# Performance work log

Hardware: AMD Instinct MI355X
Metric: run time of the kernel (lower is better)

The kernel has to match this reference:

```python
import jax, jax.numpy as jnp
import numpy as np

EPS = 1e-12  # F.normalize default eps


def _wn_weight(v, g):
    # torch weight_norm(dim=0) on Conv1d weight [out, in, 1]: w = g * v / ||v||_rows
    norm = jnp.sqrt(jnp.sum(v * v, axis=1, keepdims=True))
    return v * (g[:, None] / norm)


def _l2norm(x):
    n = jnp.sqrt(jnp.sum(x * x, axis=-1, keepdims=True))
    return x / jnp.maximum(n, EPS)


def setup_inputs() -> dict:
    key = jax.random.key(0)
    ks = jax.random.split(key, 4)
    B, D, T = 16, 1024, 4096
    CD, CS = 8, 1024
    return {
        "z": jax.random.normal(ks[0], (B, D, T), dtype=jnp.float32),
        "in_proj_v": jax.random.normal(ks[1], (CD, D), dtype=jnp.float32) * 0.02,
        "in_proj_g": jnp.ones((CD,), dtype=jnp.float32),
        "in_proj_b": jnp.zeros((CD,), dtype=jnp.float32),
        "out_proj_v": jax.random.normal(ks[2], (D, CD), dtype=jnp.float32) * 0.02,
        "out_proj_g": jnp.ones((D,), dtype=jnp.float32),
        "out_proj_b": jnp.zeros((D,), dtype=jnp.float32),
        "codebook": jax.random.normal(ks[3], (CS, CD), dtype=jnp.float32),
    }


def reference(z, in_proj_v, in_proj_g, in_proj_b, out_proj_v, out_proj_g, out_proj_b, codebook):
    B, D, T = z.shape
    CD = codebook.shape[1]

    # in_proj: 1x1 weight-normed conv == per-timestep linear
    w_in = _wn_weight(in_proj_v, in_proj_g)            # [CD, D]
    z_e = jnp.einsum('od,bdt->bot', w_in, z) + in_proj_b[None, :, None]  # [B, CD, T]

    # decode_latents: cosine-distance nearest neighbor in normalized space
    enc = jnp.transpose(z_e, (0, 2, 1)).reshape(B * T, CD)  # (b t) d
    enc_n = _l2norm(enc)
    cb_n = _l2norm(codebook)
    # dist = |e|^2 - 2 e.c + |c|^2 over normalized vectors
    dist = (jnp.sum(enc_n * enc_n, axis=1, keepdims=True)
            - 2.0 * enc_n @ cb_n.T
            + jnp.sum(cb_n * cb_n, axis=1)[None, :])       # [B*T, CS]
    indices = jnp.argmax(-dist, axis=1).reshape(B, T)      # [B, T]
    z_q = jnp.transpose(codebook[indices], (0, 2, 1))      # [B, CD, T] (un-normalized codebook gather)

    # losses (reduce over dims [1,2] -> per-batch)
    sg = jax.lax.stop_gradient
    commitment_loss = jnp.mean((z_e - sg(z_q)) ** 2, axis=(1, 2))
    codebook_loss = jnp.mean((z_q - sg(z_e)) ** 2, axis=(1, 2))

    # straight-through
    z_q_st = z_e + sg(z_q - z_e)

    w_out = _wn_weight(out_proj_v, out_proj_g)          # [D, CD]
    out = jnp.einsum('dc,bct->bdt', w_out, z_q_st) + out_proj_b[None, :, None]
    return out, commitment_loss, codebook_loss, indices, z_e
```

## Files before the change

kernel.cpp:

```cpp
#include <hip/hip_runtime.h>
#include <math.h>

#define BB 16
#define DD 1024
#define TT 4096
#define CD 8
#define CS 1024

#define OFF_LOSS_C 67108864
#define OFF_LOSS_B 67108880
#define OFF_IDX    67108896
#define OFF_ZE     67174432

#define WS_WIN  0
#define WS_WOUT 8192
#define WS_CBN  16384
#define WS_CS   24576

__global__ __launch_bounds__(256) void prep_kernel(
    const float* __restrict__ in_v,
    const float* __restrict__ in_g,
    const float* __restrict__ out_v,
    const float* __restrict__ out_g,
    const float* __restrict__ cb,
    float* __restrict__ ws)
{
    __shared__ float red[256];
    __shared__ float s_in[CD];
    int tid = threadIdx.x;

    for (int o = 0; o < CD; ++o) {
        float p = 0.f;
        for (int k = tid; k < DD; k += 256) { float v = in_v[o*DD + k]; p += v*v; }
        red[tid] = p; __syncthreads();
        for (int s = 128; s > 0; s >>= 1) { if (tid < s) red[tid] += red[tid+s]; __syncthreads(); }
        if (tid == 0) s_in[o] = in_g[o] / sqrtf(red[0]);
        __syncthreads();
    }
    for (int i = tid; i < DD*CD; i += 256) {
        int d = i >> 3, o = i & 7;
        ws[WS_WIN + i] = in_v[o*DD + d] * s_in[o];
    }
    for (int d = tid; d < DD; d += 256) {
        float v[CD]; float ssq = 0.f;
        #pragma unroll
        for (int c = 0; c < CD; ++c) { v[c] = out_v[d*CD + c]; ssq += v[c]*v[c]; }
        float s = out_g[d] / sqrtf(ssq);
        #pragma unroll
        for (int c = 0; c < CD; ++c) ws[WS_WOUT + d*CD + c] = v[c]*s;
    }
    double* cs = (double*)(ws + WS_CS);
    for (int c = tid; c < CS; c += 256) {
        float v[CD]; float ssq = 0.f;
        #pragma unroll
        for (int j = 0; j < CD; ++j) { v[j] = cb[c*CD + j]; ssq += v[j]*v[j]; }
        float n = fmaxf(sqrtf(ssq), 1e-12f);
        double sq = 0.0;
        #pragma unroll
        for (int j = 0; j < CD; ++j) {
            float e = v[j] / n;
            ws[WS_CBN + c*CD + j] = e;
            sq += (double)e * (double)e;
        }
        cs[c] = sq;
    }
}

__global__ __launch_bounds__(256) void vq_main_kernel(
    const float* __restrict__ z,
    const float* __restrict__ in_b,
    const float* __restrict__ cb,
    const float* __restrict__ ws,
    float* __restrict__ outb)
{
    __shared__ float4 cbn_s[CS*2];
    __shared__ double cs_s[CS];
    __shared__ float red[4];

    int tid = threadIdx.x;
    int b = blockIdx.y;
    int t = blockIdx.x * 256 + tid;

    {
        const float4* src = (const float4*)(ws + WS_CBN);
        for (int i = tid; i < CS*2; i += 256) cbn_s[i] = src[i];
        const double* csg = (const double*)(ws + WS_CS);
        for (int i = tid; i < CS; i += 256) cs_s[i] = csg[i];
    }
    __syncthreads();

    float acc[CD];
    #pragma unroll
    for (int o = 0; o < CD; ++o) acc[o] = in_b[o];
    const float* zp = z + (size_t)b * DD * TT + t;
    const float* w = ws + WS_WIN;
    #pragma unroll 8
    for (int d = 0; d < DD; ++d) {
        float zv = zp[(size_t)d * TT];
        #pragma unroll
        for (int o = 0; o < CD; ++o) acc[o] = fmaf(w[d*CD + o], zv, acc[o]);
    }

    #pragma unroll
    for (int o = 0; o < CD; ++o)
        outb[OFF_ZE + ((size_t)(b*CD + o)) * TT + t] = acc[o];

    float ssq = 0.f;
    #pragma unroll
    for (int o = 0; o < CD; ++o) ssq += acc[o]*acc[o];
    float nrm = fmaxf(sqrtf(ssq), 1e-12f);
    double en[CD];
    #pragma unroll
    for (int o = 0; o < CD; ++o) en[o] = (double)(acc[o] / nrm);

    double best = -1.0e300; int bidx = 0;
    for (int c = 0; c < CS; ++c) {
        float4 r0 = cbn_s[2*c], r1 = cbn_s[2*c+1];
        double dot = 0.0;
        dot = fma((double)r0.x, en[0], dot);
        dot = fma((double)r0.y, en[1], dot);
        dot = fma((double)r0.z, en[2], dot);
        dot = fma((double)r0.w, en[3], dot);
        dot = fma((double)r1.x, en[4], dot);
        dot = fma((double)r1.y, en[5], dot);
        dot = fma((double)r1.z, en[6], dot);
        dot = fma((double)r1.w, en[7], dot);
        double score = 2.0*dot - cs_s[c];
        if (score > best) { best = score; bidx = c; }
    }
    outb[OFF_IDX + b*TT + t] = (float)bidx;

    float l = 0.f;
    const float4* qr = (const float4*)(cb + bidx*CD);
    float4 q0 = qr[0], q1 = qr[1];
    {
        float dlt;
        dlt = acc[0]-q0.x; l = fmaf(dlt,dlt,l);
        dlt = acc[1]-q0.y; l = fmaf(dlt,dlt,l);
        dlt = acc[2]-q0.z; l = fmaf(dlt,dlt,l);
        dlt = acc[3]-q0.w; l = fmaf(dlt,dlt,l);
        dlt = acc[4]-q1.x; l = fmaf(dlt,dlt,l);
        dlt = acc[5]-q1.y; l = fmaf(dlt,dlt,l);
        dlt = acc[6]-q1.z; l = fmaf(dlt,dlt,l);
        dlt = acc[7]-q1.w; l = fmaf(dlt,dlt,l);
    }
    #pragma unroll
    for (int off = 32; off > 0; off >>= 1) l += __shfl_down(l, off, 64);
    if ((tid & 63) == 0) red[tid >> 6] = l;
    __syncthreads();
    if (tid == 0) {
        float s = ((red[0]+red[1]) + (red[2]+red[3])) * (1.0f/(CD*TT));
        atomicAdd(outb + OFF_LOSS_C + b, s);
        atomicAdd(outb + OFF_LOSS_B + b, s);
    }
}

__global__ __launch_bounds__(256) void out_proj_kernel(
    const float* __restrict__ cb,
    const float* __restrict__ out_b,
    const float* __restrict__ ws,
    float* __restrict__ outb)
{
    __shared__ float4 wout_s[DD*2];
    __shared__ __align__(16) float zq_s[CD][128];
    __shared__ float bias_s[DD];

    int tid = threadIdx.x;
    int b = blockIdx.y;
    int t0 = blockIdx.x * 128;

    const float4* wsrc = (const float4*)(ws + WS_WOUT);
    for (int i = tid; i < DD*2; i += 256) wout_s[i] = wsrc[i];
    for (int i = tid; i < DD; i += 256) bias_s[i] = out_b[i];
    if (tid < 128) {
        int idx = (int)outb[OFF_IDX + b*TT + t0 + tid];
        const float4* cr = (const float4*)(cb + idx*CD);
        float4 q0 = cr[0], q1 = cr[1];
        zq_s[0][tid] = q0.x; zq_s[1][tid] = q0.y; zq_s[2][tid] = q0.z; zq_s[3][tid] = q0.w;
        zq_s[4][tid] = q1.x; zq_s[5][tid] = q1.y; zq_s[6][tid] = q1.z; zq_s[7][tid] = q1.w;
    }
    __syncthreads();

    int tq = tid & 31;
    int dg = tid >> 5;
    float4 qv[CD];
    #pragma unroll
    for (int c = 0; c < CD; ++c) qv[c] = *(const float4*)&zq_s[c][tq*4];

    size_t obase = (size_t)b * DD * TT + t0 + tq*4;
    #pragma unroll 4
    for (int i = 0; i < 128; ++i) {
        int d = i*8 + dg;
        float4 w0 = wout_s[2*d], w1 = wout_s[2*d+1];
        float bb = bias_s[d];
        float4 r = make_float4(bb, bb, bb, bb);
        r.x = fmaf(w0.x, qv[0].x, r.x); r.y = fmaf(w0.x, qv[0].y, r.y); r.z = fmaf(w0.x, qv[0].z, r.z); r.w = fmaf(w0.x, qv[0].w, r.w);
        r.x = fmaf(w0.y, qv[1].x, r.x); r.y = fmaf(w0.y, qv[1].y, r.y); r.z = fmaf(w0.y, qv[1].z, r.z); r.w = fmaf(w0.y, qv[1].w, r.w);
        r.x = fmaf(w0.z, qv[2].x, r.x); r.y = fmaf(w0.z, qv[2].y, r.y); r.z = fmaf(w0.z, qv[2].z, r.z); r.w = fmaf(w0.z, qv[2].w, r.w);
        r.x = fmaf(w0.w, qv[3].x, r.x); r.y = fmaf(w0.w, qv[3].y, r.y); r.z = fmaf(w0.w, qv[3].z, r.z); r.w = fmaf(w0.w, qv[3].w, r.w);
        r.x = fmaf(w1.x, qv[4].x, r.x); r.y = fmaf(w1.x, qv[4].y, r.y); r.z = fmaf(w1.x, qv[4].z, r.z); r.w = fmaf(w1.x, qv[4].w, r.w);
        r.x = fmaf(w1.y, qv[5].x, r.x); r.y = fmaf(w1.y, qv[5].y, r.y); r.z = fmaf(w1.y, qv[5].z, r.z); r.w = fmaf(w1.y, qv[5].w, r.w);
        r.x = fmaf(w1.z, qv[6].x, r.x); r.y = fmaf(w1.z, qv[6].y, r.y); r.z = fmaf(w1.z, qv[6].z, r.z); r.w = fmaf(w1.z, qv[6].w, r.w);
        r.x = fmaf(w1.w, qv[7].x, r.x); r.y = fmaf(w1.w, qv[7].y, r.y); r.z = fmaf(w1.w, qv[7].w, r.w); r.w = fmaf(w1.w, qv[7].w, r.w);
        *(float4*)(outb + obase + (size_t)d * TT) = r;
    }
}

extern "C" void kernel_launch(void* const* d_in, const int* in_sizes, int n_in,
                              void* d_out, int out_size, void* d_ws, size_t ws_size,
                              hipStream_t stream) {
    const float* z     = (const float*)d_in[0];
    const float* in_v  = (const float*)d_in[1];
    const float* in_g  = (const float*)d_in[2];
    const float* in_b  = (const float*)d_in[3];
    const float* out_v = (const float*)d_in[4];
    const float* out_g = (const float*)d_in[5];
    const float* out_b = (const float*)d_in[6];
    const float* cb    = (const float*)d_in[7];
    float* ws  = (float*)d_ws;
    float* out = (float*)d_out;

    hipMemsetAsync(out + OFF_LOSS_C, 0, 32 * sizeof(float), stream);

    prep_kernel<<<1, 256, 0, stream>>>(in_v, in_g, out_v, out_g, cb, ws);
    vq_main_kernel<<<dim3(TT/256, BB), 256, 0, stream>>>(z, in_b, cb, ws, out);
    out_proj_kernel<<<dim3(TT/128, BB), 256, 0, stream>>>(cb, out_b, ws, out);
}
```

Before: 609.5 us.

## Split VQ projection and codebook search across waves; parallelize prep and out_proj

The VQ kernel now assigns 64 timesteps per block. Each of 4 waves reduces a quarter of the input channels, then searches a quarter of the codebook, and the partial results are merged through shared memory. This quadruples block count and shortens each thread's serial chains, improving latency hiding on the 256MB z read and the fp64 argmax scan. The prep kernel is spread over 16 blocks, and out_proj uses smaller tiles reading weights directly from global/cache instead of staging them in LDS, which also fixes a misplaced fma in the last column. Costs are extra synchronization and shared-memory partial sums.

```diff
diff --git a/kernel.cpp b/kernel.cpp
--- a/kernel.cpp
+++ b/kernel.cpp
@@ -25,32 +25,31 @@
     const float* __restrict__ cb,
     float* __restrict__ ws)
 {
-    __shared__ float red[256];
-    __shared__ float s_in[CD];
-    int tid = threadIdx.x;
-
-    for (int o = 0; o < CD; ++o) {
+    int bid = blockIdx.x, tid = threadIdx.x;
+    if (bid < 8) {
+        __shared__ float red[256];
+        __shared__ float ssc;
+        int o = bid;
         float p = 0.f;
         for (int k = tid; k < DD; k += 256) { float v = in_v[o*DD + k]; p += v*v; }
         red[tid] = p; __syncthreads();
         for (int s = 128; s > 0; s >>= 1) { if (tid < s) red[tid] += red[tid+s]; __syncthreads(); }
-        if (tid == 0) s_in[o] = in_g[o] / sqrtf(red[0]);
+        if (tid == 0) ssc = in_g[o] / sqrtf(red[0]);
         __syncthreads();
-    }
-    for (int i = tid; i < DD*CD; i += 256) {
-        int d = i >> 3, o = i & 7;
-        ws[WS_WIN + i] = in_v[o*DD + d] * s_in[o];
-    }
-    for (int d = tid; d < DD; d += 256) {
+        float scale = ssc;
+        for (int d = tid; d < DD; d += 256)
+            ws[WS_WIN + d*CD + o] = in_v[o*DD + d] * scale;
+    } else if (bid < 12) {
+        int d = (bid - 8) * 256 + tid;
         float v[CD]; float ssq = 0.f;
         #pragma unroll
         for (int c = 0; c < CD; ++c) { v[c] = out_v[d*CD + c]; ssq += v[c]*v[c]; }
         float s = out_g[d] / sqrtf(ssq);
         #pragma unroll
         for (int c = 0; c < CD; ++c) ws[WS_WOUT + d*CD + c] = v[c]*s;
-    }
-    double* cs = (double*)(ws + WS_CS);
-    for (int c = tid; c < CS; c += 256) {
+    } else {
+        int c = (bid - 12) * 256 + tid;
+        double* csh = (double*)(ws + WS_CS);
         float v[CD]; float ssq = 0.f;
         #pragma unroll
         for (int j = 0; j < CD; ++j) { v[j] = cb[c*CD + j]; ssq += v[j]*v[j]; }
@@ -60,98 +59,109 @@
         for (int j = 0; j < CD; ++j) {
             float e = v[j] / n;
             ws[WS_CBN + c*CD + j] = e;
-            sq += (double)e * (double)e;
-        }
-        cs[c] = sq;
-    }
-}
-
-__global__ __launch_bounds__(256) void vq_main_kernel(
+            sq = fma((double)e, (double)e, sq);
+        }
+        csh[c] = 0.5 * sq;
+    }
+}
+
+__global__ __launch_bounds__(256) void vq_kernel(
     const float* __restrict__ z,
     const float* __restrict__ in_b,
     const float* __restrict__ cb,
     const float* __restrict__ ws,
     float* __restrict__ outb)
 {
-    __shared__ float4 cbn_s[CS*2];
-    __shared__ double cs_s[CS];
-    __shared__ float red[4];
+    __shared__ float  zpart[4][CD][64];
+    __shared__ float  ze_s[CD][64];
+    __shared__ float  nrm_s[64];
+    __shared__ double best_s[4][64];
+    __shared__ int    bidx_s[4][64];
 
     int tid = threadIdx.x;
-    int b = blockIdx.y;
-    int t = blockIdx.x * 256 + tid;
+    int b   = blockIdx.y;
+    int t0  = blockIdx.x * 64;
+    int tl  = tid & 63;
+    int wv  = __builtin_amdgcn_readfirstlane(tid >> 6);
+
+    const float* zp = z + ((size_t)(b*DD + wv*256)) * TT + t0 + tl;
+    const float* w  = ws + WS_WIN + wv*256*CD;
+    float acc[CD];
+    #pragma unroll
+    for (int o = 0; o < CD; ++o) acc[o] = 0.f;
+    #pragma unroll 8
+    for (int j = 0; j < 256; ++j) {
+        float zv = zp[(size_t)j * TT];
+        #pragma unroll
+        for (int o = 0; o < CD; ++o) acc[o] = fmaf(w[j*CD + o], zv, acc[o]);
+    }
+    #pragma unroll
+    for (int o = 0; o < CD; ++o) zpart[wv][o][tl] = acc[o];
+    __syncthreads();
+
+    #pragma unroll
+    for (int p = tid; p < 512; p += 256) {
+        int o = p >> 6, t = p & 63;
+        float v = in_b[o] + ((zpart[0][o][t] + zpart[1][o][t]) +
+                             (zpart[2][o][t] + zpart[3][o][t]));
+        ze_s[o][t] = v;
+        outb[OFF_ZE + ((size_t)(b*CD + o)) * TT + t0 + t] = v;
+    }
+    __syncthreads();
+    if (tid < 64) {
+        float ssq = 0.f;
+        #pragma unroll
+        for (int o = 0; o < CD; ++o) { float v = ze_s[o][tid]; ssq = fmaf(v, v, ssq); }
+        nrm_s[tid] = fmaxf(sqrtf(ssq), 1e-12f);
+    }
+    __syncthreads();
 
     {
-        const float4* src = (const float4*)(ws + WS_CBN);
-        for (int i = tid; i < CS*2; i += 256) cbn_s[i] = src[i];
-        const double* csg = (const double*)(ws + WS_CS);
-        for (int i = tid; i < CS; i += 256) cs_s[i] = csg[i];
-    }
-    __syncthreads();
-
-    float acc[CD];
-    #pragma unroll
-    for (int o = 0; o < CD; ++o) acc[o] = in_b[o];
-    const float* zp = z + (size_t)b * DD * TT + t;
-    const float* w = ws + WS_WIN;
-    #pragma unroll 8
-    for (int d = 0; d < DD; ++d) {
-        float zv = zp[(size_t)d * TT];
-        #pragma unroll
-        for (int o = 0; o < CD; ++o) acc[o] = fmaf(w[d*CD + o], zv, acc[o]);
-    }
-
-    #pragma unroll
-    for (int o = 0; o < CD; ++o)
-        outb[OFF_ZE + ((size_t)(b*CD + o)) * TT + t] = acc[o];
-
-    float ssq = 0.f;
-    #pragma unroll
-    for (int o = 0; o < CD; ++o) ssq += acc[o]*acc[o];
-    float nrm = fmaxf(sqrtf(ssq), 1e-12f);
-    double en[CD];
-    #pragma unroll
-    for (int o = 0; o < CD; ++o) en[o] = (double)(acc[o] / nrm);
-
-    double best = -1.0e300; int bidx = 0;
-    for (int c = 0; c < CS; ++c) {
-        float4 r0 = cbn_s[2*c], r1 = cbn_s[2*c+1];
-        double dot = 0.0;
-        dot = fma((double)r0.x, en[0], dot);
-        dot = fma((double)r0.y, en[1], dot);
-        dot = fma((double)r0.z, en[2], dot);
-        dot = fma((double)r0.w, en[3], dot);
-        dot = fma((double)r1.x, en[4], dot);
-        dot = fma((double)r1.y, en[5], dot);
-        dot = fma((double)r1.z, en[6], dot);
-        dot = fma((double)r1.w, en[7], dot);
-        double score = 2.0*dot - cs_s[c];
-        if (score > best) { best = score; bidx = c; }
-    }
-    outb[OFF_IDX + b*TT + t] = (float)bidx;
-
-    float l = 0.f;
-    const float4* qr = (const float4*)(cb + bidx*CD);
-    float4 q0 = qr[0], q1 = qr[1];
-    {
-        float dlt;
-        dlt = acc[0]-q0.x; l = fmaf(dlt,dlt,l);
-        dlt = acc[1]-q0.y; l = fmaf(dlt,dlt,l);
-        dlt = acc[2]-q0.z; l = fmaf(dlt,dlt,l);
-        dlt = acc[3]-q0.w; l = fmaf(dlt,dlt,l);
-        dlt = acc[4]-q1.x; l = fmaf(dlt,dlt,l);
-        dlt = acc[5]-q1.y; l = fmaf(dlt,dlt,l);
-        dlt = acc[6]-q1.z; l = fmaf(dlt,dlt,l);
-        dlt = acc[7]-q1.w; l = fmaf(dlt,dlt,l);
-    }
-    #pragma unroll
-    for (int off = 32; off > 0; off >>= 1) l += __shfl_down(l, off, 64);
-    if ((tid & 63) == 0) red[tid >> 6] = l;
-    __syncthreads();
-    if (tid == 0) {
-        float s = ((red[0]+red[1]) + (red[2]+red[3])) * (1.0f/(CD*TT));
-        atomicAdd(outb + OFF_LOSS_C + b, s);
-        atomicAdd(outb + OFF_LOSS_B + b, s);
+        int t = tl;
+        float nr = nrm_s[t];
+        double en[CD];
+        #pragma unroll
+        for (int o = 0; o < CD; ++o) en[o] = (double)(ze_s[o][t] / nr);
+        const float*  cbn = ws + WS_CBN;
+        const double* csh = (const double*)(ws + WS_CS);
+        int c0 = wv * 256;
+        double best = -1.0e300; int bi = c0;
+        for (int c = c0; c < c0 + 256; ++c) {
+            float cr[CD];
+            *(float4*)&cr[0] = *(const float4*)(cbn + c*CD);
+            *(float4*)&cr[4] = *(const float4*)(cbn + c*CD + 4);
+            double dot = 0.0;
+            #pragma unroll
+            for (int o = 0; o < CD; ++o) dot = fma((double)cr[o], en[o], dot);
+            double score = dot - csh[c];
+            if (score > best) { best = score; bi = c; }
+        }
+        best_s[wv][t] = best; bidx_s[wv][t] = bi;
+    }
+    __syncthreads();
+
+    if (tid < 64) {
+        int t = tid;
+        double best = best_s[0][t]; int bi = bidx_s[0][t];
+        #pragma unroll
+        for (int k = 1; k < 4; ++k) {
+            if (best_s[k][t] > best) { best = best_s[k][t]; bi = bidx_s[k][t]; }
+        }
+        outb[OFF_IDX + b*TT + t0 + t] = (float)bi;
+
+        float q[CD];
+        *(float4*)&q[0] = *(const float4*)(cb + bi*CD);
+        *(float4*)&q[4] = *(const float4*)(cb + bi*CD + 4);
+        float l = 0.f;
+        #pragma unroll
+        for (int o = 0; o < CD; ++o) { float d = ze_s[o][t] - q[o]; l = fmaf(d, d, l); }
+        #pragma unroll
+        for (int off = 32; off > 0; off >>= 1) l += __shfl_down(l, off, 64);
+        if (tid == 0) {
+            float s = l * (1.0f / (CD * TT));
+            atomicAdd(outb + OFF_LOSS_C + b, s);
+            atomicAdd(outb + OFF_LOSS_B + b, s);
+        }
     }
 }
 
@@ -161,47 +171,45 @@
     const float* __restrict__ ws,
     float* __restrict__ outb)
 {
-    __shared__ float4 wout_s[DD*2];
-    __shared__ __align__(16) float zq_s[CD][128];
-    __shared__ float bias_s[DD];
+    __shared__ __align__(16) float zq_s[CD][64];
 
     int tid = threadIdx.x;
-    int b = blockIdx.y;
-    int t0 = blockIdx.x * 128;
-
-    const float4* wsrc = (const float4*)(ws + WS_WOUT);
-    for (int i = tid; i < DD*2; i += 256) wout_s[i] = wsrc[i];
-    for (int i = tid; i < DD; i += 256) bias_s[i] = out_b[i];
-    if (tid < 128) {
-        int idx = (int)outb[OFF_IDX + b*TT + t0 + tid];
-        const float4* cr = (const float4*)(cb + idx*CD);
+    int b   = blockIdx.y;
+    int t0  = blockIdx.x * 64;
+
+    if (tid < 64) {
+        int bi = (int)outb[OFF_IDX + b*TT + t0 + tid];
+        const float4* cr = (const float4*)(cb + bi*CD);
         float4 q0 = cr[0], q1 = cr[1];
         zq_s[0][tid] = q0.x; zq_s[1][tid] = q0.y; zq_s[2][tid] = q0.z; zq_s[3][tid] = q0.w;
         zq_s[4][tid] = q1.x; zq_s[5][tid] = q1.y; zq_s[6][tid] = q1.z; zq_s[7][tid] = q1.w;
     }
     __syncthreads();
 
-    int tq = tid & 31;
-    int dg = tid >> 5;
+    int tq = tid & 15;
+    int dg = tid >> 4;
     float4 qv[CD];
     #pragma unroll
-    for (int c = 0; c < CD; ++c) qv[c] = *(const float4*)&zq_s[c][tq*4];
+    for (int o = 0; o < CD; ++o) qv[o] = *(const float4*)&zq_s[o][tq*4];
 
     size_t obase = (size_t)b * DD * TT + t0 + tq*4;
+    const float4* wv4 = (const float4*)(ws + WS_WOUT);
     #pragma unroll 4
-    for (int i = 0; i < 128; ++i) {
-        int d = i*8 + dg;
-        float4 w0 = wout_s[2*d], w1 = wout_s[2*d+1];
-        float bb = bias_s[d];
+    for (int i = 0; i < 64; ++i) {
+        int d = i*16 + dg;
+        float wr[CD];
+        *(float4*)&wr[0] = wv4[2*d];
+        *(float4*)&wr[4] = wv4[2*d + 1];
+        float bb = out_b[d];
         float4 r = make_float4(bb, bb, bb, bb);
-        r.x = fmaf(w0.x, qv[0].x, r.x); r.y = fmaf(w0.x, qv[0].y, r.y); r.z = fmaf(w0.x, qv[0].z, r.z); r.w = fmaf(w0.x, qv[0].w, r.w);
-        r.x = fmaf(w0.y, qv[1].x, r.x); r.y = fmaf(w0.y, qv[1].y, r.y); r.z = fmaf(w0.y, qv[1].z, r.z); r.w = fmaf(w0.y, qv[1].w, r.w);
-        r.x = fmaf(w0.z, qv[2].x, r.x); r.y = fmaf(w0.z, qv[2].y, r.y); r.z = fmaf(w0.z, qv[2].z, r.z); r.w = fmaf(w0.z, qv[2].w, r.w);
-        r.x = fmaf(w0.w, qv[3].x, r.x); r.y = fmaf(w0.w, qv[3].y, r.y); r.z = fmaf(w0.w, qv[3].z, r.z); r.w = fmaf(w0.w, qv[3].w, r.w);
-        r.x = fmaf(w1.x, qv[4].x, r.x); r.y = fmaf(w1.x, qv[4].y, r.y); r.z = fmaf(w1.x, qv[4].z, r.z); r.w = fmaf(w1.x, qv[4].w, r.w);
-        r.x = fmaf(w1.y, qv[5].x, r.x); r.y = fmaf(w1.y, qv[5].y, r.y); r.z = fmaf(w1.y, qv[5].z, r.z); r.w = fmaf(w1.y, qv[5].w, r.w);
-        r.x = fmaf(w1.z, qv[6].x, r.x); r.y = fmaf(w1.z, qv[6].y, r.y); r.z = fmaf(w1.z, qv[6].z, r.z); r.w = fmaf(w1.z, qv[6].w, r.w);
-        r.x = fmaf(w1.w, qv[7].x, r.x); r.y = fmaf(w1.w, qv[7].y, r.y); r.z = fmaf(w1.w, qv[7].w, r.w); r.w = fmaf(w1.w, qv[7].w, r.w);
+        #pragma unroll
+        for (int o = 0; o < CD; ++o) {
+            float wo = wr[o];
+            r.x = fmaf(wo, qv[o].x, r.x);
+            r.y = fmaf(wo, qv[o].y, r.y);
+            r.z = fmaf(wo, qv[o].z, r.z);
+            r.w = fmaf(wo, qv[o].w, r.w);
+        }
         *(float4*)(outb + obase + (size_t)d * TT) = r;
     }
 }
@@ -222,7 +230,7 @@
 
     hipMemsetAsync(out + OFF_LOSS_C, 0, 32 * sizeof(float), stream);
 
-    prep_kernel<<<1, 256, 0, stream>>>(in_v, in_g, out_v, out_g, cb, ws);
-    vq_main_kernel<<<dim3(TT/256, BB), 256, 0, stream>>>(z, in_b, cb, ws, out);
-    out_proj_kernel<<<dim3(TT/128, BB), 256, 0, stream>>>(cb, out_b, ws, out);
-}
+    prep_kernel<<<16, 256, 0, stream>>>(in_v, in_g, out_v, out_g, cb, ws);
+    vq_kernel<<<dim3(TT/64, BB), 256, 0, stream>>>(z, in_b, cb, ws, out);
+    out_proj_kernel<<<dim3(TT/64, BB), 256, 0, stream>>>(cb, out_b, ws, out);
+}
```

Result: faster. 587.0 us (-3.7%).
